# Optimization experiments

Measured on AMD Instinct MI355X. Metric: run time of the kernel, lower is better.

Reference implementation:

```python
import jax, jax.numpy as jnp
import numpy as np

B, T, D = 64, 4096, 256
UNITS = 256

def setup_inputs() -> dict:
    key = jax.random.key(0)
    k0, k1, k2, k3 = jax.random.split(key, 4)
    lstm_output = jax.random.normal(k0, (B, T, D), dtype=jnp.float32)
    # Glorot-ish scaled dense weights (no bias per module)
    W1 = jax.random.normal(k1, (D, UNITS), dtype=jnp.float32) * (1.0 / np.sqrt(D))
    W2 = jax.random.normal(k2, (D, UNITS), dtype=jnp.float32) * (1.0 / np.sqrt(D))
    v = jax.random.normal(k3, (UNITS, 1), dtype=jnp.float32) * (1.0 / np.sqrt(UNITS))
    return {"lstm_output": lstm_output, "W1": W1, "W2": W2, "v": v}

def reference(lstm_output, W1, W2, v):
    # query/key: [B, T, units]
    query = jnp.einsum("btd,du->btu", lstm_output, W1)
    key = jnp.einsum("btd,du->btu", lstm_output, W2)
    # score: [B, T, 1]
    score = jnp.einsum("btu,uo->bto", jnp.tanh(query + key), v)
    # softmax over time axis (axis=1)
    attention_weights = jax.nn.softmax(score, axis=1)
    # context: [B, D]
    context_vector = jnp.sum(attention_weights * lstm_output, axis=1)
    return (context_vector, attention_weights)
```

## Files before the change

kernel.cpp:

```cpp
#include <hip/hip_runtime.h>
#include <math.h>

#define B 64
#define T 4096
#define D 256
#define U 256

typedef __attribute__((ext_vector_type(8)))  short s16x8;
typedef __attribute__((ext_vector_type(16))) float f32x16;

#define MT 32
#define SPB 16
#define NBLK ((B*T)/(MT*SPB))
#define LDAP 33

#define TCH 128
#define NCH (T / TCH)

#define DPP_ADD(v, ctrl)                                                     \
  v += __int_as_float(__builtin_amdgcn_update_dpp(                           \
      0, __float_as_int(v), ctrl, 0xF, 0xF, true))

__global__ __launch_bounds__(512, 2) void scores_mfma_kernel(
    const float* __restrict__ A,
    const float* __restrict__ W1,
    const float* __restrict__ W2,
    const float* __restrict__ v,
    float* __restrict__ s_out)
{
  __shared__ uint4 AH[32 * LDAP];
  __shared__ uint4 AL[32 * LDAP];
  __shared__ float red[32][8];

  const int tid  = threadIdx.x;
  const int lane = tid & 63;
  const int wv   = tid >> 6;
  const int l31  = lane & 31;
  const int half = lane >> 5;

  const int n = wv * 32 + l31;
  s16x8 Bh[16], Bl[16];
#pragma unroll
  for (int s = 0; s < 16; ++s) {
    s16x8 bh, bl;
#pragma unroll
    for (int j = 0; j < 8; ++j) {
      const int k = s * 16 + half * 8 + j;
      const float w = W1[k * 256 + n] + W2[k * 256 + n];
      const unsigned int uw = __float_as_uint(w);
      const float wl = w - __uint_as_float(uw & 0xffff0000u);
      bh[j] = (short)(uw >> 16);
      bl[j] = (short)(__float_as_uint(wl) >> 16);
    }
    Bh[s] = bh; Bl[s] = bl;
  }
  const float vv = v[n];

  const int sm  = tid >> 4;
  const int sc0 = tid & 15;

  const size_t row0 = (size_t)blockIdx.x * (MT * SPB);
  float4 rg[4];
  {
    const float4* src = (const float4*)(A + (row0 + sm) * 256);
#pragma unroll
    for (int i = 0; i < 4; ++i) rg[i] = src[sc0 + 16 * i];
  }

  for (int step = 0; step < SPB; ++step) {
    const size_t rowbase = row0 + (size_t)step * MT;

#pragma unroll
    for (int i = 0; i < 4; ++i) {
      const float4 a = rg[i];
      const int k  = 4 * (sc0 + 16 * i);
      const int k8 = k >> 3;
      const int off = (k >> 2) & 1;
      const unsigned int ux = __float_as_uint(a.x), uy = __float_as_uint(a.y);
      const unsigned int uz = __float_as_uint(a.z), uw = __float_as_uint(a.w);
      const uint2 hi2 = make_uint2((ux >> 16) | (uy & 0xffff0000u),
                                   (uz >> 16) | (uw & 0xffff0000u));
      const float lx = a.x - __uint_as_float(ux & 0xffff0000u);
      const float ly = a.y - __uint_as_float(uy & 0xffff0000u);
      const float lz = a.z - __uint_as_float(uz & 0xffff0000u);
      const float lw = a.w - __uint_as_float(uw & 0xffff0000u);
      const uint2 lo2 = make_uint2(
          (__float_as_uint(lx) >> 16) | (__float_as_uint(ly) & 0xffff0000u),
          (__float_as_uint(lz) >> 16) | (__float_as_uint(lw) & 0xffff0000u));
      ((uint2*)&AH[k8 * LDAP + sm])[off] = hi2;
      ((uint2*)&AL[k8 * LDAP + sm])[off] = lo2;
    }
    __syncthreads();

    if (step + 1 < SPB) {
      const float4* src = (const float4*)(A + (rowbase + MT + sm) * 256);
#pragma unroll
      for (int i = 0; i < 4; ++i) rg[i] = src[sc0 + 16 * i];
    }

    f32x16 a0 = {}, a1 = {}, a2 = {};
#pragma unroll
    for (int s = 0; s < 16; ++s) {
      const uint4 qh = AH[(2 * s + half) * LDAP + l31];
      const uint4 ql = AL[(2 * s + half) * LDAP + l31];
      const s16x8 ah = __builtin_bit_cast(s16x8, qh);
      const s16x8 al = __builtin_bit_cast(s16x8, ql);
      a0 = __builtin_amdgcn_mfma_f32_32x32x16_bf16(ah, Bh[s], a0, 0, 0, 0);
      a1 = __builtin_amdgcn_mfma_f32_32x32x16_bf16(ah, Bl[s], a1, 0, 0, 0);
      a2 = __builtin_amdgcn_mfma_f32_32x32x16_bf16(al, Bh[s], a2, 0, 0, 0);
    }

#pragma unroll
    for (int r = 0; r < 16; ++r) {
      const float x = a0[r] + a1[r] + a2[r];
      const float e = __expf(x + x);
      float p = (1.f - 2.f * __builtin_amdgcn_rcpf(e + 1.f)) * vv;
      DPP_ADD(p, 0xB1);
      DPP_ADD(p, 0x4E);
      DPP_ADD(p, 0x141);
      DPP_ADD(p, 0x140);
      p += __int_as_float(
          __builtin_amdgcn_ds_swizzle(__float_as_int(p), 0x401F));
      if (l31 == 0)
        red[(r & 3) + 8 * (r >> 2) + 4 * half][wv] = p;
    }
    __syncthreads();

    if (tid < 32) {
      const float4* rp = (const float4*)&red[tid][0];
      const float4 ra = rp[0], rb = rp[1];
      s_out[rowbase + tid] = ra.x + ra.y + ra.z + ra.w + rb.x + rb.y + rb.z + rb.w;
    }
  }
}

__global__ __launch_bounds__(1024) void softmax_kernel(float* __restrict__ attn) {
    const int b = blockIdx.x;
    float* row = attn + (long)b * T;
    const int tid = threadIdx.x;
    const int wave = tid >> 6, lane = tid & 63;

    __shared__ float lmax[16];
    __shared__ float lsum[16];
    __shared__ float bcast[2];

    float4 s = ((const float4*)row)[tid];
    float m = fmaxf(fmaxf(s.x, s.y), fmaxf(s.z, s.w));
    for (int off = 32; off > 0; off >>= 1) m = fmaxf(m, __shfl_down(m, off));
    if (lane == 0) lmax[wave] = m;
    __syncthreads();
    if (tid == 0) {
        float mm = lmax[0];
        for (int i = 1; i < 16; ++i) mm = fmaxf(mm, lmax[i]);
        bcast[0] = mm;
    }
    __syncthreads();
    m = bcast[0];

    float4 e;
    e.x = expf(s.x - m); e.y = expf(s.y - m);
    e.z = expf(s.z - m); e.w = expf(s.w - m);
    float sum = e.x + e.y + e.z + e.w;
    for (int off = 32; off > 0; off >>= 1) sum += __shfl_down(sum, off);
    if (lane == 0) lsum[wave] = sum;
    __syncthreads();
    if (tid == 0) {
        float ss = 0.f;
        for (int i = 0; i < 16; ++i) ss += lsum[i];
        bcast[1] = 1.0f / ss;
    }
    __syncthreads();
    const float inv = bcast[1];
    e.x *= inv; e.y *= inv; e.z *= inv; e.w *= inv;
    ((float4*)row)[tid] = e;
}

__global__ __launch_bounds__(256, 4) void context_partial_kernel(
    const float* __restrict__ A, const float* __restrict__ attn,
    float* __restrict__ part)
{
    const int chunk = blockIdx.x;
    const int b = blockIdx.y;
    const int tg = threadIdx.x >> 6;
    const int l = threadIdx.x & 63;
    const int dl = l * 4;
    const long tokbase = (long)b * T + (long)chunk * TCH + (long)tg * 32;

    const float4* wp = (const float4*)(attn + tokbase);
    float4 acc = make_float4(0.f, 0.f, 0.f, 0.f);
#pragma unroll
    for (int t8 = 0; t8 < 32; t8 += 8) {
        const float4 wa = wp[t8 / 4];
        const float4 wb = wp[t8 / 4 + 1];
        float w[8];
        *(float4*)&w[0] = wa;
        *(float4*)&w[4] = wb;
#pragma unroll
        for (int j = 0; j < 8; ++j) {
            const float4 x = *(const float4*)(A + (tokbase + t8 + j) * 256 + dl);
            acc.x = fmaf(w[j], x.x, acc.x);
            acc.y = fmaf(w[j], x.y, acc.y);
            acc.z = fmaf(w[j], x.z, acc.z);
            acc.w = fmaf(w[j], x.w, acc.w);
        }
    }

    __shared__ float4 red[4][64];
    red[tg][l] = acc;
    __syncthreads();
    if (tg == 0) {
        float4 r = red[0][l];
        const float4 r1 = red[1][l], r2 = red[2][l], r3 = red[3][l];
        r.x += r1.x + r2.x + r3.x;
        r.y += r1.y + r2.y + r3.y;
        r.z += r1.z + r2.z + r3.z;
        r.w += r1.w + r2.w + r3.w;
        float* p = part + ((long)chunk * B + b) * D + dl;
        p[0] = r.x; p[1] = r.y; p[2] = r.z; p[3] = r.w;
    }
}

__global__ void context_reduce_kernel(const float* __restrict__ part,
                                      float* __restrict__ ctx) {
    const int i = blockIdx.x * 256 + threadIdx.x;
    float s = 0.f;
    for (int c = 0; c < NCH; ++c) s += part[(long)c * (B * D) + i];
    ctx[i] = s;
}

extern "C" void kernel_launch(void* const* d_in, const int* in_sizes, int n_in,
                              void* d_out, int out_size, void* d_ws, size_t ws_size,
                              hipStream_t stream) {
    const float* lstm = (const float*)d_in[0];
    const float* W1   = (const float*)d_in[1];
    const float* W2   = (const float*)d_in[2];
    const float* v    = (const float*)d_in[3];

    float* out  = (float*)d_out;
    float* ctx  = out;
    float* attn = out + B * D;

    float* part = (float*)d_ws;

    scores_mfma_kernel<<<NBLK, 512, 0, stream>>>(lstm, W1, W2, v, attn);
    softmax_kernel<<<B, 1024, 0, stream>>>(attn);
    context_partial_kernel<<<dim3(NCH, B), 256, 0, stream>>>(lstm, attn, part);
    context_reduce_kernel<<<(B * D) / 256, 256, 0, stream>>>(part, ctx);
}
```

Before: 436.7 us.

## Fuse context accumulation into score kernel with unnormalized softmax weights

The score kernel now computes exp(score) with no max subtraction and accumulates the weighted context sum from the bf16 hi/lo tiles already in shared memory. It also accumulates per-block partial normalizers. A small finalize kernel divides by the summed normalizer to produce both the attention weights and the context vector, which removes the second full read of the input and the separate softmax and reduce launches. Skipping max subtraction risks overflow for large scores, and the context is rebuilt from the split-bf16 representation rather than the original fp32 values.

```diff
diff --git a/kernel.cpp b/kernel.cpp
--- a/kernel.cpp
+++ b/kernel.cpp
@@ -14,23 +14,37 @@
 #define NBLK ((B*T)/(MT*SPB))
 #define LDAP 33
 
-#define TCH 128
-#define NCH (T / TCH)
-
 #define DPP_ADD(v, ctrl)                                                     \
   v += __int_as_float(__builtin_amdgcn_update_dpp(                           \
       0, __float_as_int(v), ctrl, 0xF, 0xF, true))
 
-__global__ __launch_bounds__(512, 2) void scores_mfma_kernel(
+__device__ __forceinline__ void acc8(float* acc, float wr, uint4 h, uint4 l) {
+  const unsigned* hw = (const unsigned*)&h;
+  const unsigned* lw = (const unsigned*)&l;
+#pragma unroll
+  for (int jw = 0; jw < 4; ++jw) {
+    const float ae = __uint_as_float(hw[jw] << 16) +
+                     __uint_as_float(lw[jw] << 16);
+    const float ao = __uint_as_float(hw[jw] & 0xffff0000u) +
+                     __uint_as_float(lw[jw] & 0xffff0000u);
+    acc[2 * jw]     = fmaf(wr, ae, acc[2 * jw]);
+    acc[2 * jw + 1] = fmaf(wr, ao, acc[2 * jw + 1]);
+  }
+}
+
+__global__ __launch_bounds__(512, 2) void scores_ctx_kernel(
     const float* __restrict__ A,
     const float* __restrict__ W1,
     const float* __restrict__ W2,
     const float* __restrict__ v,
-    float* __restrict__ s_out)
+    float* __restrict__ w_out,
+    float* __restrict__ part,
+    float* __restrict__ zpart)
 {
   __shared__ uint4 AH[32 * LDAP];
   __shared__ uint4 AL[32 * LDAP];
   __shared__ float red[32][8];
+  __shared__ float wbuf[32];
 
   const int tid  = threadIdx.x;
   const int lane = tid & 63;
@@ -58,6 +72,12 @@
 
   const int sm  = tid >> 4;
   const int sc0 = tid & 15;
+
+  const int k8c = tid >> 4;
+  const int mlc = tid & 15;
+
+  float acc[8] = {0.f, 0.f, 0.f, 0.f, 0.f, 0.f, 0.f, 0.f};
+  float zacc = 0.f;
 
   const size_t row0 = (size_t)blockIdx.x * (MT * SPB);
   float4 rg[4];
@@ -129,103 +149,82 @@
     if (tid < 32) {
       const float4* rp = (const float4*)&red[tid][0];
       const float4 ra = rp[0], rb = rp[1];
-      s_out[rowbase + tid] = ra.x + ra.y + ra.z + ra.w + rb.x + rb.y + rb.z + rb.w;
-    }
-  }
-}
-
-__global__ __launch_bounds__(1024) void softmax_kernel(float* __restrict__ attn) {
-    const int b = blockIdx.x;
-    float* row = attn + (long)b * T;
-    const int tid = threadIdx.x;
-    const int wave = tid >> 6, lane = tid & 63;
-
-    __shared__ float lmax[16];
-    __shared__ float lsum[16];
-    __shared__ float bcast[2];
-
-    float4 s = ((const float4*)row)[tid];
-    float m = fmaxf(fmaxf(s.x, s.y), fmaxf(s.z, s.w));
-    for (int off = 32; off > 0; off >>= 1) m = fmaxf(m, __shfl_down(m, off));
-    if (lane == 0) lmax[wave] = m;
-    __syncthreads();
-    if (tid == 0) {
-        float mm = lmax[0];
-        for (int i = 1; i < 16; ++i) mm = fmaxf(mm, lmax[i]);
-        bcast[0] = mm;
-    }
-    __syncthreads();
-    m = bcast[0];
-
-    float4 e;
-    e.x = expf(s.x - m); e.y = expf(s.y - m);
-    e.z = expf(s.z - m); e.w = expf(s.w - m);
-    float sum = e.x + e.y + e.z + e.w;
-    for (int off = 32; off > 0; off >>= 1) sum += __shfl_down(sum, off);
-    if (lane == 0) lsum[wave] = sum;
-    __syncthreads();
-    if (tid == 0) {
-        float ss = 0.f;
-        for (int i = 0; i < 16; ++i) ss += lsum[i];
-        bcast[1] = 1.0f / ss;
-    }
-    __syncthreads();
-    const float inv = bcast[1];
-    e.x *= inv; e.y *= inv; e.z *= inv; e.w *= inv;
-    ((float4*)row)[tid] = e;
-}
-
-__global__ __launch_bounds__(256, 4) void context_partial_kernel(
-    const float* __restrict__ A, const float* __restrict__ attn,
-    float* __restrict__ part)
+      const float s =
+          ra.x + ra.y + ra.z + ra.w + rb.x + rb.y + rb.z + rb.w;
+      const float w = __expf(s);
+      w_out[rowbase + tid] = w;
+      wbuf[tid] = w;
+      zacc += w;
+    }
+    __syncthreads();
+
+    {
+      const float w0 = wbuf[mlc];
+      const float w1 = wbuf[mlc + 16];
+      const uint4 h0 = AH[k8c * LDAP + mlc];
+      const uint4 l0 = AL[k8c * LDAP + mlc];
+      const uint4 h1 = AH[k8c * LDAP + mlc + 16];
+      const uint4 l1 = AL[k8c * LDAP + mlc + 16];
+      acc8(acc, w0, h0, l0);
+      acc8(acc, w1, h1, l1);
+    }
+    __syncthreads();
+  }
+
+  float accsel = 0.f;
+#pragma unroll
+  for (int j = 0; j < 8; ++j) {
+    float p = acc[j];
+    DPP_ADD(p, 0xB1);
+    DPP_ADD(p, 0x4E);
+    DPP_ADD(p, 0x141);
+    DPP_ADD(p, 0x140);
+    if ((tid & 15) == j) accsel = p;
+  }
+  if ((tid & 15) < 8)
+    part[blockIdx.x * 256 + k8c * 8 + (tid & 15)] = accsel;
+
+  if (tid < 32) {
+    float z = zacc;
+    DPP_ADD(z, 0xB1);
+    DPP_ADD(z, 0x4E);
+    DPP_ADD(z, 0x141);
+    DPP_ADD(z, 0x140);
+    z += __int_as_float(
+        __builtin_amdgcn_ds_swizzle(__float_as_int(z), 0x401F));
+    if (tid == 0) zpart[blockIdx.x] = z;
+  }
+}
+
+__global__ __launch_bounds__(1024) void finalize_kernel(
+    const float* __restrict__ part,
+    const float* __restrict__ zpart,
+    float* __restrict__ attn,
+    float* __restrict__ ctx)
 {
-    const int chunk = blockIdx.x;
-    const int b = blockIdx.y;
-    const int tg = threadIdx.x >> 6;
-    const int l = threadIdx.x & 63;
-    const int dl = l * 4;
-    const long tokbase = (long)b * T + (long)chunk * TCH + (long)tg * 32;
-
-    const float4* wp = (const float4*)(attn + tokbase);
-    float4 acc = make_float4(0.f, 0.f, 0.f, 0.f);
-#pragma unroll
-    for (int t8 = 0; t8 < 32; t8 += 8) {
-        const float4 wa = wp[t8 / 4];
-        const float4 wb = wp[t8 / 4 + 1];
-        float w[8];
-        *(float4*)&w[0] = wa;
-        *(float4*)&w[4] = wb;
-#pragma unroll
-        for (int j = 0; j < 8; ++j) {
-            const float4 x = *(const float4*)(A + (tokbase + t8 + j) * 256 + dl);
-            acc.x = fmaf(w[j], x.x, acc.x);
-            acc.y = fmaf(w[j], x.y, acc.y);
-            acc.z = fmaf(w[j], x.z, acc.z);
-            acc.w = fmaf(w[j], x.w, acc.w);
-        }
-    }
-
-    __shared__ float4 red[4][64];
-    red[tg][l] = acc;
-    __syncthreads();
-    if (tg == 0) {
-        float4 r = red[0][l];
-        const float4 r1 = red[1][l], r2 = red[2][l], r3 = red[3][l];
-        r.x += r1.x + r2.x + r3.x;
-        r.y += r1.y + r2.y + r3.y;
-        r.z += r1.z + r2.z + r3.z;
-        r.w += r1.w + r2.w + r3.w;
-        float* p = part + ((long)chunk * B + b) * D + dl;
-        p[0] = r.x; p[1] = r.y; p[2] = r.z; p[3] = r.w;
-    }
-}
-
-__global__ void context_reduce_kernel(const float* __restrict__ part,
-                                      float* __restrict__ ctx) {
-    const int i = blockIdx.x * 256 + threadIdx.x;
+  const int b = blockIdx.x;
+  const int tid = threadIdx.x;
+  __shared__ float shinv;
+  if (tid == 0) {
+    float z = 0.f;
+#pragma unroll
+    for (int c = 0; c < 8; ++c) z += zpart[b * 8 + c];
+    shinv = 1.0f / z;
+  }
+  __syncthreads();
+  const float iz = shinv;
+
+  if (tid < D) {
     float s = 0.f;
-    for (int c = 0; c < NCH; ++c) s += part[(long)c * (B * D) + i];
-    ctx[i] = s;
+#pragma unroll
+    for (int c = 0; c < 8; ++c) s += part[(b * 8 + c) * D + tid];
+    ctx[b * D + tid] = s * iz;
+  }
+
+  float4* row = (float4*)(attn + (long)b * T);
+  float4 w4 = row[tid];
+  w4.x *= iz; w4.y *= iz; w4.z *= iz; w4.w *= iz;
+  row[tid] = w4;
 }
 
 extern "C" void kernel_launch(void* const* d_in, const int* in_sizes, int n_in,
@@ -240,10 +239,9 @@
     float* ctx  = out;
     float* attn = out + B * D;
 
-    float* part = (float*)d_ws;
-
-    scores_mfma_kernel<<<NBLK, 512, 0, stream>>>(lstm, W1, W2, v, attn);
-    softmax_kernel<<<B, 1024, 0, stream>>>(attn);
-    context_partial_kernel<<<dim3(NCH, B), 256, 0, stream>>>(lstm, attn, part);
-    context_reduce_kernel<<<(B * D) / 256, 256, 0, stream>>>(part, ctx);
-}
+    float* part  = (float*)d_ws;
+    float* zpart = part + NBLK * D;
+
+    scores_ctx_kernel<<<NBLK, 512, 0, stream>>>(lstm, W1, W2, v, attn, part, zpart);
+    finalize_kernel<<<B, 1024, 0, stream>>>(part, zpart, attn, ctx);
+}
```

Measured after the change: 414.5 us. 5.1% less time.
